# Performance work log

Hardware: AMD Instinct MI355X
Metric: run time of the kernel (lower is better)

## Reference

```python
import jax, jax.numpy as jnp
import numpy as np

B, T, D, H = 1024, 200, 128, 128


def setup_inputs() -> dict:
    key = jax.random.key(0)
    k1, k2, k3, k4 = jax.random.split(key, 4)
    item_his_eb = jax.random.normal(k1, (B, T, D), dtype=jnp.float32)
    seq_len = jax.random.randint(k2, (B,), 0, T, dtype=jnp.int32)
    # TF GRUCell packs [r, u] gates in one matmul over concat([x, h]).
    W_gate = jax.random.normal(k3, (D + H, 2 * H), dtype=jnp.float32) * (1.0 / np.sqrt(D + H))
    b_gate = jnp.ones((2 * H,), dtype=jnp.float32)  # TF GRUCell bias init = 1.0
    W_cand = jax.random.normal(k4, (D + H, H), dtype=jnp.float32) * (1.0 / np.sqrt(D + H))
    b_cand = jnp.zeros((H,), dtype=jnp.float32)
    return {"item_his_eb": item_his_eb, "seq_len": seq_len,
            "W_gate": W_gate, "b_gate": b_gate,
            "W_cand": W_cand, "b_cand": b_cand}


def reference(item_his_eb, seq_len, W_gate, b_gate, W_cand, b_cand):
    # dynamic_rnn(GRUCell(H)) with sequence_length masking.
    # Outputs are zero and state is held for steps t >= seq_len.
    Bq, Tq, Dq = item_his_eb.shape
    Hq = W_cand.shape[1]
    x_tbd = jnp.transpose(item_his_eb, (1, 0, 2))  # [T, B, D]

    def step(h, inp):
        x_t, t = inp  # x_t: [B, D], t: scalar int
        gates = jax.nn.sigmoid(jnp.concatenate([x_t, h], axis=-1) @ W_gate + b_gate)
        r, u = jnp.split(gates, 2, axis=-1)  # each [B, H]
        c = jnp.tanh(jnp.concatenate([x_t, r * h], axis=-1) @ W_cand + b_cand)
        h_new = u * h + (1.0 - u) * c
        valid = (t < seq_len)[:, None]  # [B, 1]
        h_next = jnp.where(valid, h_new, h)
        y = jnp.where(valid, h_new, jnp.zeros_like(h_new))
        return h_next, y

    h0 = jnp.zeros((Bq, Hq), dtype=item_his_eb.dtype)
    _, ys = jax.lax.scan(step, h0, (x_tbd, jnp.arange(Tq)))
    return jnp.transpose(ys, (1, 0, 2))  # [B, T, H]
```

## Files before the change

### kernel.cpp

```cpp
#include <hip/hip_runtime.h>

#define T_SZ 200
#define H_SZ 128

typedef __attribute__((ext_vector_type(8))) short    bf16x8;
typedef __attribute__((ext_vector_type(4))) float    f32x4;
typedef __attribute__((ext_vector_type(4))) int      i32x4;
typedef __attribute__((ext_vector_type(2))) unsigned u32x2;

__device__ __forceinline__ unsigned short f2bf(float f) {
  unsigned u = __builtin_bit_cast(unsigned, f);
  u += 0x7fffu + ((u >> 16) & 1u);
  return (unsigned short)(u >> 16);
}
__device__ __forceinline__ unsigned cvt_pk_bf16(float a, float b) {
  unsigned r;
  asm("v_cvt_pk_bf16_f32 %0, %1, %2" : "=v"(r) : "v"(a), "v"(b));
  return r;
}
__device__ __forceinline__ float sigmoid_fast(float x) {
  float e = __builtin_amdgcn_exp2f(-1.442695041f * x);
  return __builtin_amdgcn_rcpf(1.0f + e);
}
__device__ __forceinline__ float tanh_fast(float x) {
  float e = __builtin_amdgcn_exp2f(2.885390082f * x);
  return 1.0f - 2.0f * __builtin_amdgcn_rcpf(e + 1.0f);
}
__device__ __forceinline__ void ldsbar() {
  __asm__ __volatile__("" ::: "memory");
  __builtin_amdgcn_s_waitcnt(0xc07f);
  __builtin_amdgcn_s_barrier();
  __asm__ __volatile__("" ::: "memory");
}

__global__ __launch_bounds__(512, 1) void gru_fused(
    const float* __restrict__ X,
    const int*   __restrict__ seq_len,
    const float* __restrict__ Wg,
    const float* __restrict__ bg,
    const float* __restrict__ Wc,
    const float* __restrict__ bc,
    float* __restrict__ Y)
{
  __shared__ unsigned short hA[16 * 136];
  __shared__ unsigned short rhA[16 * 136];
  __shared__ unsigned short xA[2][16 * 136];

  const int tid  = threadIdx.x;
  const int lane = tid & 63;
  const int w    = tid >> 6;
  const int m16  = lane & 15;
  const int q    = lane >> 4;

  bf16x8 wgf[2][8];
  float  gbias[2];
  #pragma unroll
  for (int nt = 0; nt < 2; ++nt) {
    int col = nt * 128 + w * 16 + m16;
    gbias[nt] = bg[col];
    #pragma unroll
    for (int kb = 0; kb < 8; ++kb) {
      bf16x8 f;
      #pragma unroll
      for (int j = 0; j < 8; ++j)
        f[j] = (short)f2bf(Wg[(size_t)(kb * 32 + q * 8 + j) * 256 + col]);
      wgf[nt][kb] = f;
    }
  }
  const int colc = w * 16 + m16;
  bf16x8 wcf[8];
  float  cbias = bc[colc];
  #pragma unroll
  for (int kb = 0; kb < 8; ++kb) {
    bf16x8 f;
    #pragma unroll
    for (int j = 0; j < 8; ++j)
      f[j] = (short)f2bf(Wc[(size_t)(kb * 32 + q * 8 + j) * 128 + colc]);
    wcf[kb] = f;
  }

  const int bt = blockIdx.x;
  int slen[4];
  #pragma unroll
  for (int i = 0; i < 4; ++i) slen[i] = seq_len[bt * 16 + q * 4 + i];

  float h[4] = {0.f, 0.f, 0.f, 0.f};

  for (int idx = tid; idx < 16 * 136; idx += 512) hA[idx] = 0;

  const int xrow = tid >> 5;
  const int xk4  = (tid & 31) * 4;
  const float* xbase = X + (size_t)(bt * 16 + xrow) * T_SZ * 128 + xk4;

  auto xload = [&](int t, f32x4& r) {
    r = *(const f32x4*)(xbase + (size_t)t * 128);
  };
  auto xstage = [&](int buf, const f32x4& r) {
    unsigned d0 = cvt_pk_bf16(r.x, r.y);
    unsigned d1 = cvt_pk_bf16(r.z, r.w);
    *(u32x2*)&xA[buf][xrow * 136 + xk4] = (u32x2){d0, d1};
  };

  f32x4 x0r, x1r, xrE, xrO;
  xload(0, x0r); xload(1, x1r);
  xstage(0, x0r); xstage(1, x1r);
  xload(2, xrE); xload(3, xrO);
  ldsbar();

  f32x4 axrA, axuA, ccA, axrB, axuB, ccB;
  {
    bf16x8 xaf[4];
    #pragma unroll
    for (int kb = 0; kb < 4; ++kb)
      xaf[kb] = __builtin_bit_cast(bf16x8, *(const i32x4*)&xA[0][m16 * 136 + kb * 32 + q * 8]);
    f32x4 cc = { cbias, cbias, cbias, cbias };
    f32x4 ar = { gbias[0], gbias[0], gbias[0], gbias[0] };
    f32x4 au = { gbias[1], gbias[1], gbias[1], gbias[1] };
    #pragma unroll
    for (int kb = 0; kb < 4; ++kb) {
      cc = __builtin_amdgcn_mfma_f32_16x16x32_bf16(xaf[kb], wcf[kb],    cc, 0, 0, 0);
      ar = __builtin_amdgcn_mfma_f32_16x16x32_bf16(xaf[kb], wgf[0][kb], ar, 0, 0, 0);
      au = __builtin_amdgcn_mfma_f32_16x16x32_bf16(xaf[kb], wgf[1][kb], au, 0, 0, 0);
    }
    ccA = cc; axrA = ar; axuA = au;
  }
  ldsbar();

  float* const ybase = Y + (size_t)(bt * 16 + q * 4) * T_SZ * H_SZ + colc;

  auto step = [&](int t, f32x4& xreg,
                  f32x4& axin_r, f32x4& axin_u, f32x4& ccin,
                  f32x4& axout_r, f32x4& axout_u, f32x4& ccout) {
    bf16x8 haf[4];
    #pragma unroll
    for (int kb = 0; kb < 4; ++kb)
      haf[kb] = __builtin_bit_cast(bf16x8, *(const i32x4*)&hA[m16 * 136 + kb * 32 + q * 8]);

    if (t < 198) xstage(t & 1, xreg);
    if (t < 196) xload(t + 4, xreg);

    f32x4 ra = axin_r, rb = { 0.f, 0.f, 0.f, 0.f };
    ra = __builtin_amdgcn_mfma_f32_16x16x32_bf16(haf[0], wgf[0][4], ra, 0, 0, 0);
    ra = __builtin_amdgcn_mfma_f32_16x16x32_bf16(haf[1], wgf[0][5], ra, 0, 0, 0);
    rb = __builtin_amdgcn_mfma_f32_16x16x32_bf16(haf[2], wgf[0][6], rb, 0, 0, 0);
    rb = __builtin_amdgcn_mfma_f32_16x16x32_bf16(haf[3], wgf[0][7], rb, 0, 0, 0);

    float rh0 = sigmoid_fast(ra[0] + rb[0]) * h[0];
    float rh1 = sigmoid_fast(ra[1] + rb[1]) * h[1];
    float rh2 = sigmoid_fast(ra[2] + rb[2]) * h[2];
    float rh3 = sigmoid_fast(ra[3] + rb[3]) * h[3];
    unsigned rp01 = cvt_pk_bf16(rh0, rh1);
    unsigned rp23 = cvt_pk_bf16(rh2, rh3);
    rhA[(q * 4 + 0) * 136 + colc] = (unsigned short)(rp01 & 0xffffu);
    rhA[(q * 4 + 1) * 136 + colc] = (unsigned short)(rp01 >> 16);
    rhA[(q * 4 + 2) * 136 + colc] = (unsigned short)(rp23 & 0xffffu);
    rhA[(q * 4 + 3) * 136 + colc] = (unsigned short)(rp23 >> 16);
    ldsbar();

    bf16x8 rhf[4];
    #pragma unroll
    for (int kb = 0; kb < 4; ++kb)
      rhf[kb] = __builtin_bit_cast(bf16x8, *(const i32x4*)&rhA[m16 * 136 + kb * 32 + q * 8]);
    bf16x8 xaf2[4];
    if (t < 199) {
      const unsigned short* xb = xA[(t + 1) & 1];
      #pragma unroll
      for (int kb = 0; kb < 4; ++kb)
        xaf2[kb] = __builtin_bit_cast(bf16x8, *(const i32x4*)&xb[m16 * 136 + kb * 32 + q * 8]);
    }

    f32x4 ua = axin_u, ub = { 0.f, 0.f, 0.f, 0.f };
    ua = __builtin_amdgcn_mfma_f32_16x16x32_bf16(haf[0], wgf[1][4], ua, 0, 0, 0);
    ua = __builtin_amdgcn_mfma_f32_16x16x32_bf16(haf[1], wgf[1][5], ua, 0, 0, 0);
    ub = __builtin_amdgcn_mfma_f32_16x16x32_bf16(haf[2], wgf[1][6], ub, 0, 0, 0);
    ub = __builtin_amdgcn_mfma_f32_16x16x32_bf16(haf[3], wgf[1][7], ub, 0, 0, 0);

    f32x4 ca = ccin, cb = { 0.f, 0.f, 0.f, 0.f };
    ca = __builtin_amdgcn_mfma_f32_16x16x32_bf16(rhf[0], wcf[4], ca, 0, 0, 0);
    ca = __builtin_amdgcn_mfma_f32_16x16x32_bf16(rhf[1], wcf[5], ca, 0, 0, 0);
    cb = __builtin_amdgcn_mfma_f32_16x16x32_bf16(rhf[2], wcf[6], cb, 0, 0, 0);
    cb = __builtin_amdgcn_mfma_f32_16x16x32_bf16(rhf[3], wcf[7], cb, 0, 0, 0);

    if (t < 199) {
      f32x4 cc = { cbias, cbias, cbias, cbias };
      f32x4 ar = { gbias[0], gbias[0], gbias[0], gbias[0] };
      f32x4 au = { gbias[1], gbias[1], gbias[1], gbias[1] };
      #pragma unroll
      for (int kb = 0; kb < 4; ++kb) {
        cc = __builtin_amdgcn_mfma_f32_16x16x32_bf16(xaf2[kb], wcf[kb],    cc, 0, 0, 0);
        ar = __builtin_amdgcn_mfma_f32_16x16x32_bf16(xaf2[kb], wgf[0][kb], ar, 0, 0, 0);
        au = __builtin_amdgcn_mfma_f32_16x16x32_bf16(xaf2[kb], wgf[1][kb], au, 0, 0, 0);
      }
      ccout = cc; axout_r = ar; axout_u = au;
    }

    f32x4 uv;
    #pragma unroll
    for (int i = 0; i < 4; ++i) uv[i] = sigmoid_fast(ua[i] + ub[i]);

    #pragma unroll
    for (int i = 0; i < 4; ++i) {
      float c  = tanh_fast(ca[i] + cb[i]);
      float hn = uv[i] * (h[i] - c) + c;
      bool valid = (t < slen[i]);
      float hvz = valid ? hn : h[i];
      h[i] = hvz;
      ybase[(size_t)i * T_SZ * H_SZ + (size_t)t * H_SZ] = valid ? hn : 0.0f;
    }
    unsigned hp01 = cvt_pk_bf16(h[0], h[1]);
    unsigned hp23 = cvt_pk_bf16(h[2], h[3]);
    hA[(q * 4 + 0) * 136 + colc] = (unsigned short)(hp01 & 0xffffu);
    hA[(q * 4 + 1) * 136 + colc] = (unsigned short)(hp01 >> 16);
    hA[(q * 4 + 2) * 136 + colc] = (unsigned short)(hp23 & 0xffffu);
    hA[(q * 4 + 3) * 136 + colc] = (unsigned short)(hp23 >> 16);
    ldsbar();
  };

  for (int t = 0; t < 200; t += 2) {
    step(t,     xrE, axrA, axuA, ccA, axrB, axuB, ccB);
    step(t + 1, xrO, axrB, axuB, ccB, axrA, axuA, ccA);
  }
}

extern "C" void kernel_launch(void* const* d_in, const int* in_sizes, int n_in,
                              void* d_out, int out_size, void* d_ws, size_t ws_size,
                              hipStream_t stream) {
  const float* X   = (const float*)d_in[0];
  const int*   seq = (const int*)  d_in[1];
  const float* Wg  = (const float*)d_in[2];
  const float* bg  = (const float*)d_in[3];
  const float* Wc  = (const float*)d_in[4];
  const float* bc  = (const float*)d_in[5];
  float* Y = (float*)d_out;
  (void)d_ws; (void)ws_size;

  hipLaunchKernelGGL(gru_fused, dim3(64), dim3(512), 0, stream,
                     X, seq, Wg, bg, Wc, bc, Y);
}
```

Baseline: 334.2 us.

## Load X directly into MFMA fragment registers, dropping LDS staging

Each lane now reads its own MFMA A-fragment of X straight from global memory, prefetching two steps ahead, and converts it to bf16 in registers. This removes the shared-memory x buffers, the per-step LDS store and load of x, and the ping-pong accumulator sets. The update-gate accumulation is also merged into one chain instead of two partial sums. In exchange, global loads are no longer coalesced across rows (each lane reads 32-byte pieces), each thread holds more registers for the prefetched X, and the update-gate MFMA chain is longer and more serial.

```diff
diff --git a/kernel.cpp b/kernel.cpp
--- a/kernel.cpp
+++ b/kernel.cpp
@@ -6,7 +6,6 @@
 typedef __attribute__((ext_vector_type(8))) short    bf16x8;
 typedef __attribute__((ext_vector_type(4))) float    f32x4;
 typedef __attribute__((ext_vector_type(4))) int      i32x4;
-typedef __attribute__((ext_vector_type(2))) unsigned u32x2;
 
 __device__ __forceinline__ unsigned short f2bf(float f) {
   unsigned u = __builtin_bit_cast(unsigned, f);
@@ -44,7 +43,6 @@
 {
   __shared__ unsigned short hA[16 * 136];
   __shared__ unsigned short rhA[16 * 136];
-  __shared__ unsigned short xA[2][16 * 136];
 
   const int tid  = threadIdx.x;
   const int lane = tid & 63;
@@ -88,58 +86,58 @@
 
   for (int idx = tid; idx < 16 * 136; idx += 512) hA[idx] = 0;
 
-  const int xrow = tid >> 5;
-  const int xk4  = (tid & 31) * 4;
-  const float* xbase = X + (size_t)(bt * 16 + xrow) * T_SZ * 128 + xk4;
-
-  auto xload = [&](int t, f32x4& r) {
-    r = *(const f32x4*)(xbase + (size_t)t * 128);
+  const float* const xrow = X + (size_t)(bt * 16 + m16) * T_SZ * 128 + q * 8;
+  f32x4 xf[8];
+  auto xissue = [&](int t) {
+    const float* p = xrow + (size_t)t * 128;
+    #pragma unroll
+    for (int kb = 0; kb < 4; ++kb) {
+      xf[2 * kb]     = *(const f32x4*)(p + kb * 32);
+      xf[2 * kb + 1] = *(const f32x4*)(p + kb * 32 + 4);
+    }
   };
-  auto xstage = [&](int buf, const f32x4& r) {
-    unsigned d0 = cvt_pk_bf16(r.x, r.y);
-    unsigned d1 = cvt_pk_bf16(r.z, r.w);
-    *(u32x2*)&xA[buf][xrow * 136 + xk4] = (u32x2){d0, d1};
+
+  f32x4 axr, axu, cc;
+
+  auto xproj = [&]() {
+    bf16x8 xbf[4];
+    #pragma unroll
+    for (int kb = 0; kb < 4; ++kb) {
+      i32x4 pk = { (int)cvt_pk_bf16(xf[2 * kb].x,     xf[2 * kb].y),
+                   (int)cvt_pk_bf16(xf[2 * kb].z,     xf[2 * kb].w),
+                   (int)cvt_pk_bf16(xf[2 * kb + 1].x, xf[2 * kb + 1].y),
+                   (int)cvt_pk_bf16(xf[2 * kb + 1].z, xf[2 * kb + 1].w) };
+      xbf[kb] = __builtin_bit_cast(bf16x8, pk);
+    }
+    f32x4 c_ = { cbias, cbias, cbias, cbias };
+    f32x4 r_ = { gbias[0], gbias[0], gbias[0], gbias[0] };
+    f32x4 u_ = { gbias[1], gbias[1], gbias[1], gbias[1] };
+    #pragma unroll
+    for (int kb = 0; kb < 4; ++kb) {
+      c_ = __builtin_amdgcn_mfma_f32_16x16x32_bf16(xbf[kb], wcf[kb],    c_, 0, 0, 0);
+      r_ = __builtin_amdgcn_mfma_f32_16x16x32_bf16(xbf[kb], wgf[0][kb], r_, 0, 0, 0);
+      u_ = __builtin_amdgcn_mfma_f32_16x16x32_bf16(xbf[kb], wgf[1][kb], u_, 0, 0, 0);
+    }
+    cc = c_; axr = r_; axu = u_;
   };
 
-  f32x4 x0r, x1r, xrE, xrO;
-  xload(0, x0r); xload(1, x1r);
-  xstage(0, x0r); xstage(1, x1r);
-  xload(2, xrE); xload(3, xrO);
+  xissue(0);
   ldsbar();
-
-  f32x4 axrA, axuA, ccA, axrB, axuB, ccB;
   {
-    bf16x8 xaf[4];
-    #pragma unroll
-    for (int kb = 0; kb < 4; ++kb)
-      xaf[kb] = __builtin_bit_cast(bf16x8, *(const i32x4*)&xA[0][m16 * 136 + kb * 32 + q * 8]);
-    f32x4 cc = { cbias, cbias, cbias, cbias };
-    f32x4 ar = { gbias[0], gbias[0], gbias[0], gbias[0] };
-    f32x4 au = { gbias[1], gbias[1], gbias[1], gbias[1] };
-    #pragma unroll
-    for (int kb = 0; kb < 4; ++kb) {
-      cc = __builtin_amdgcn_mfma_f32_16x16x32_bf16(xaf[kb], wcf[kb],    cc, 0, 0, 0);
-      ar = __builtin_amdgcn_mfma_f32_16x16x32_bf16(xaf[kb], wgf[0][kb], ar, 0, 0, 0);
-      au = __builtin_amdgcn_mfma_f32_16x16x32_bf16(xaf[kb], wgf[1][kb], au, 0, 0, 0);
-    }
-    ccA = cc; axrA = ar; axuA = au;
-  }
-  ldsbar();
+    bf16x8 dummy_guard;  (void)dummy_guard;
+  }
+  xproj();
+  xissue(1);
 
   float* const ybase = Y + (size_t)(bt * 16 + q * 4) * T_SZ * H_SZ + colc;
 
-  auto step = [&](int t, f32x4& xreg,
-                  f32x4& axin_r, f32x4& axin_u, f32x4& ccin,
-                  f32x4& axout_r, f32x4& axout_u, f32x4& ccout) {
+  for (int t = 0; t < 200; ++t) {
     bf16x8 haf[4];
     #pragma unroll
     for (int kb = 0; kb < 4; ++kb)
       haf[kb] = __builtin_bit_cast(bf16x8, *(const i32x4*)&hA[m16 * 136 + kb * 32 + q * 8]);
 
-    if (t < 198) xstage(t & 1, xreg);
-    if (t < 196) xload(t + 4, xreg);
-
-    f32x4 ra = axin_r, rb = { 0.f, 0.f, 0.f, 0.f };
+    f32x4 ra = axr, rb = { 0.f, 0.f, 0.f, 0.f };
     ra = __builtin_amdgcn_mfma_f32_16x16x32_bf16(haf[0], wgf[0][4], ra, 0, 0, 0);
     ra = __builtin_amdgcn_mfma_f32_16x16x32_bf16(haf[1], wgf[0][5], ra, 0, 0, 0);
     rb = __builtin_amdgcn_mfma_f32_16x16x32_bf16(haf[2], wgf[0][6], rb, 0, 0, 0);
@@ -161,42 +159,27 @@
     #pragma unroll
     for (int kb = 0; kb < 4; ++kb)
       rhf[kb] = __builtin_bit_cast(bf16x8, *(const i32x4*)&rhA[m16 * 136 + kb * 32 + q * 8]);
-    bf16x8 xaf2[4];
-    if (t < 199) {
-      const unsigned short* xb = xA[(t + 1) & 1];
-      #pragma unroll
-      for (int kb = 0; kb < 4; ++kb)
-        xaf2[kb] = __builtin_bit_cast(bf16x8, *(const i32x4*)&xb[m16 * 136 + kb * 32 + q * 8]);
-    }
-
-    f32x4 ua = axin_u, ub = { 0.f, 0.f, 0.f, 0.f };
+
+    f32x4 ua = axu;
     ua = __builtin_amdgcn_mfma_f32_16x16x32_bf16(haf[0], wgf[1][4], ua, 0, 0, 0);
     ua = __builtin_amdgcn_mfma_f32_16x16x32_bf16(haf[1], wgf[1][5], ua, 0, 0, 0);
-    ub = __builtin_amdgcn_mfma_f32_16x16x32_bf16(haf[2], wgf[1][6], ub, 0, 0, 0);
-    ub = __builtin_amdgcn_mfma_f32_16x16x32_bf16(haf[3], wgf[1][7], ub, 0, 0, 0);
-
-    f32x4 ca = ccin, cb = { 0.f, 0.f, 0.f, 0.f };
+    ua = __builtin_amdgcn_mfma_f32_16x16x32_bf16(haf[2], wgf[1][6], ua, 0, 0, 0);
+    ua = __builtin_amdgcn_mfma_f32_16x16x32_bf16(haf[3], wgf[1][7], ua, 0, 0, 0);
+
+    f32x4 ca = cc, cb = { 0.f, 0.f, 0.f, 0.f };
     ca = __builtin_amdgcn_mfma_f32_16x16x32_bf16(rhf[0], wcf[4], ca, 0, 0, 0);
     ca = __builtin_amdgcn_mfma_f32_16x16x32_bf16(rhf[1], wcf[5], ca, 0, 0, 0);
     cb = __builtin_amdgcn_mfma_f32_16x16x32_bf16(rhf[2], wcf[6], cb, 0, 0, 0);
     cb = __builtin_amdgcn_mfma_f32_16x16x32_bf16(rhf[3], wcf[7], cb, 0, 0, 0);
 
     if (t < 199) {
-      f32x4 cc = { cbias, cbias, cbias, cbias };
-      f32x4 ar = { gbias[0], gbias[0], gbias[0], gbias[0] };
-      f32x4 au = { gbias[1], gbias[1], gbias[1], gbias[1] };
-      #pragma unroll
-      for (int kb = 0; kb < 4; ++kb) {
-        cc = __builtin_amdgcn_mfma_f32_16x16x32_bf16(xaf2[kb], wcf[kb],    cc, 0, 0, 0);
-        ar = __builtin_amdgcn_mfma_f32_16x16x32_bf16(xaf2[kb], wgf[0][kb], ar, 0, 0, 0);
-        au = __builtin_amdgcn_mfma_f32_16x16x32_bf16(xaf2[kb], wgf[1][kb], au, 0, 0, 0);
-      }
-      ccout = cc; axout_r = ar; axout_u = au;
+      xproj();
+      if (t < 198) xissue(t + 2);
     }
 
     f32x4 uv;
     #pragma unroll
-    for (int i = 0; i < 4; ++i) uv[i] = sigmoid_fast(ua[i] + ub[i]);
+    for (int i = 0; i < 4; ++i) uv[i] = sigmoid_fast(ua[i]);
 
     #pragma unroll
     for (int i = 0; i < 4; ++i) {
@@ -214,11 +197,6 @@
     hA[(q * 4 + 2) * 136 + colc] = (unsigned short)(hp23 & 0xffffu);
     hA[(q * 4 + 3) * 136 + colc] = (unsigned short)(hp23 >> 16);
     ldsbar();
-  };
-
-  for (int t = 0; t < 200; t += 2) {
-    step(t,     xrE, axrA, axuA, ccA, axrB, axuB, ccB);
-    step(t + 1, xrO, axrB, axuB, ccB, axrA, axuA, ccA);
   }
 }
 
```

Result: slower. 670.1 us (+100.5%).

## Swap MFMA operands so each lane owns four hidden columns of one row

Applied to the files above, without the earlier changes.

The MFMA A/B operands are swapped so the accumulator holds a transposed tile: each lane now owns four consecutive hidden columns for a single batch row, not one column across four rows. This lets the per-step h and r*h LDS writes become single 8-byte stores, the Y output a single 16-byte vector store, and seq_len a single scalar per lane. The u-gate accumulation is also folded into one chain, removing one add per element but lengthening that dependency chain. Bias loading becomes vector loads matching the new layout.

```diff
diff --git a/kernel.cpp b/kernel.cpp
--- a/kernel.cpp
+++ b/kernel.cpp
@@ -53,11 +53,9 @@
   const int q    = lane >> 4;
 
   bf16x8 wgf[2][8];
-  float  gbias[2];
   #pragma unroll
   for (int nt = 0; nt < 2; ++nt) {
     int col = nt * 128 + w * 16 + m16;
-    gbias[nt] = bg[col];
     #pragma unroll
     for (int kb = 0; kb < 8; ++kb) {
       bf16x8 f;
@@ -69,7 +67,6 @@
   }
   const int colc = w * 16 + m16;
   bf16x8 wcf[8];
-  float  cbias = bc[colc];
   #pragma unroll
   for (int kb = 0; kb < 8; ++kb) {
     bf16x8 f;
@@ -79,10 +76,13 @@
     wcf[kb] = f;
   }
 
+  const int col4 = w * 16 + q * 4;
+  const f32x4 gbias_r = *(const f32x4*)&bg[col4];
+  const f32x4 gbias_u = *(const f32x4*)&bg[128 + col4];
+  const f32x4 cbias4  = *(const f32x4*)&bc[col4];
+
   const int bt = blockIdx.x;
-  int slen[4];
-  #pragma unroll
-  for (int i = 0; i < 4; ++i) slen[i] = seq_len[bt * 16 + q * 4 + i];
+  const int slen = seq_len[bt * 16 + m16];
 
   float h[4] = {0.f, 0.f, 0.f, 0.f};
 
@@ -113,20 +113,18 @@
     #pragma unroll
     for (int kb = 0; kb < 4; ++kb)
       xaf[kb] = __builtin_bit_cast(bf16x8, *(const i32x4*)&xA[0][m16 * 136 + kb * 32 + q * 8]);
-    f32x4 cc = { cbias, cbias, cbias, cbias };
-    f32x4 ar = { gbias[0], gbias[0], gbias[0], gbias[0] };
-    f32x4 au = { gbias[1], gbias[1], gbias[1], gbias[1] };
+    f32x4 cc = cbias4, ar = gbias_r, au = gbias_u;
     #pragma unroll
     for (int kb = 0; kb < 4; ++kb) {
-      cc = __builtin_amdgcn_mfma_f32_16x16x32_bf16(xaf[kb], wcf[kb],    cc, 0, 0, 0);
-      ar = __builtin_amdgcn_mfma_f32_16x16x32_bf16(xaf[kb], wgf[0][kb], ar, 0, 0, 0);
-      au = __builtin_amdgcn_mfma_f32_16x16x32_bf16(xaf[kb], wgf[1][kb], au, 0, 0, 0);
+      cc = __builtin_amdgcn_mfma_f32_16x16x32_bf16(wcf[kb],    xaf[kb], cc, 0, 0, 0);
+      ar = __builtin_amdgcn_mfma_f32_16x16x32_bf16(wgf[0][kb], xaf[kb], ar, 0, 0, 0);
+      au = __builtin_amdgcn_mfma_f32_16x16x32_bf16(wgf[1][kb], xaf[kb], au, 0, 0, 0);
     }
     ccA = cc; axrA = ar; axuA = au;
   }
   ldsbar();
 
-  float* const ybase = Y + (size_t)(bt * 16 + q * 4) * T_SZ * H_SZ + colc;
+  float* const ybase = Y + (size_t)(bt * 16 + m16) * T_SZ * H_SZ + col4;
 
   auto step = [&](int t, f32x4& xreg,
                   f32x4& axin_r, f32x4& axin_u, f32x4& ccin,
@@ -140,21 +138,17 @@
     if (t < 196) xload(t + 4, xreg);
 
     f32x4 ra = axin_r, rb = { 0.f, 0.f, 0.f, 0.f };
-    ra = __builtin_amdgcn_mfma_f32_16x16x32_bf16(haf[0], wgf[0][4], ra, 0, 0, 0);
-    ra = __builtin_amdgcn_mfma_f32_16x16x32_bf16(haf[1], wgf[0][5], ra, 0, 0, 0);
-    rb = __builtin_amdgcn_mfma_f32_16x16x32_bf16(haf[2], wgf[0][6], rb, 0, 0, 0);
-    rb = __builtin_amdgcn_mfma_f32_16x16x32_bf16(haf[3], wgf[0][7], rb, 0, 0, 0);
+    ra = __builtin_amdgcn_mfma_f32_16x16x32_bf16(wgf[0][4], haf[0], ra, 0, 0, 0);
+    ra = __builtin_amdgcn_mfma_f32_16x16x32_bf16(wgf[0][5], haf[1], ra, 0, 0, 0);
+    rb = __builtin_amdgcn_mfma_f32_16x16x32_bf16(wgf[0][6], haf[2], rb, 0, 0, 0);
+    rb = __builtin_amdgcn_mfma_f32_16x16x32_bf16(wgf[0][7], haf[3], rb, 0, 0, 0);
 
     float rh0 = sigmoid_fast(ra[0] + rb[0]) * h[0];
     float rh1 = sigmoid_fast(ra[1] + rb[1]) * h[1];
     float rh2 = sigmoid_fast(ra[2] + rb[2]) * h[2];
     float rh3 = sigmoid_fast(ra[3] + rb[3]) * h[3];
-    unsigned rp01 = cvt_pk_bf16(rh0, rh1);
-    unsigned rp23 = cvt_pk_bf16(rh2, rh3);
-    rhA[(q * 4 + 0) * 136 + colc] = (unsigned short)(rp01 & 0xffffu);
-    rhA[(q * 4 + 1) * 136 + colc] = (unsigned short)(rp01 >> 16);
-    rhA[(q * 4 + 2) * 136 + colc] = (unsigned short)(rp23 & 0xffffu);
-    rhA[(q * 4 + 3) * 136 + colc] = (unsigned short)(rp23 >> 16);
+    *(u32x2*)&rhA[m16 * 136 + col4] =
+        (u32x2){ cvt_pk_bf16(rh0, rh1), cvt_pk_bf16(rh2, rh3) };
     ldsbar();
 
     bf16x8 rhf[4];
@@ -169,50 +163,42 @@
         xaf2[kb] = __builtin_bit_cast(bf16x8, *(const i32x4*)&xb[m16 * 136 + kb * 32 + q * 8]);
     }
 
-    f32x4 ua = axin_u, ub = { 0.f, 0.f, 0.f, 0.f };
-    ua = __builtin_amdgcn_mfma_f32_16x16x32_bf16(haf[0], wgf[1][4], ua, 0, 0, 0);
-    ua = __builtin_amdgcn_mfma_f32_16x16x32_bf16(haf[1], wgf[1][5], ua, 0, 0, 0);
-    ub = __builtin_amdgcn_mfma_f32_16x16x32_bf16(haf[2], wgf[1][6], ub, 0, 0, 0);
-    ub = __builtin_amdgcn_mfma_f32_16x16x32_bf16(haf[3], wgf[1][7], ub, 0, 0, 0);
+    f32x4 ua = axin_u;
+    ua = __builtin_amdgcn_mfma_f32_16x16x32_bf16(wgf[1][4], haf[0], ua, 0, 0, 0);
+    ua = __builtin_amdgcn_mfma_f32_16x16x32_bf16(wgf[1][5], haf[1], ua, 0, 0, 0);
+    ua = __builtin_amdgcn_mfma_f32_16x16x32_bf16(wgf[1][6], haf[2], ua, 0, 0, 0);
+    ua = __builtin_amdgcn_mfma_f32_16x16x32_bf16(wgf[1][7], haf[3], ua, 0, 0, 0);
 
     f32x4 ca = ccin, cb = { 0.f, 0.f, 0.f, 0.f };
-    ca = __builtin_amdgcn_mfma_f32_16x16x32_bf16(rhf[0], wcf[4], ca, 0, 0, 0);
-    ca = __builtin_amdgcn_mfma_f32_16x16x32_bf16(rhf[1], wcf[5], ca, 0, 0, 0);
-    cb = __builtin_amdgcn_mfma_f32_16x16x32_bf16(rhf[2], wcf[6], cb, 0, 0, 0);
-    cb = __builtin_amdgcn_mfma_f32_16x16x32_bf16(rhf[3], wcf[7], cb, 0, 0, 0);
+    ca = __builtin_amdgcn_mfma_f32_16x16x32_bf16(wcf[4], rhf[0], ca, 0, 0, 0);
+    ca = __builtin_amdgcn_mfma_f32_16x16x32_bf16(wcf[5], rhf[1], ca, 0, 0, 0);
+    cb = __builtin_amdgcn_mfma_f32_16x16x32_bf16(wcf[6], rhf[2], cb, 0, 0, 0);
+    cb = __builtin_amdgcn_mfma_f32_16x16x32_bf16(wcf[7], rhf[3], cb, 0, 0, 0);
 
     if (t < 199) {
-      f32x4 cc = { cbias, cbias, cbias, cbias };
-      f32x4 ar = { gbias[0], gbias[0], gbias[0], gbias[0] };
-      f32x4 au = { gbias[1], gbias[1], gbias[1], gbias[1] };
+      f32x4 cc = cbias4, ar = gbias_r, au = gbias_u;
       #pragma unroll
       for (int kb = 0; kb < 4; ++kb) {
-        cc = __builtin_amdgcn_mfma_f32_16x16x32_bf16(xaf2[kb], wcf[kb],    cc, 0, 0, 0);
-        ar = __builtin_amdgcn_mfma_f32_16x16x32_bf16(xaf2[kb], wgf[0][kb], ar, 0, 0, 0);
-        au = __builtin_amdgcn_mfma_f32_16x16x32_bf16(xaf2[kb], wgf[1][kb], au, 0, 0, 0);
+        cc = __builtin_amdgcn_mfma_f32_16x16x32_bf16(wcf[kb],    xaf2[kb], cc, 0, 0, 0);
+        ar = __builtin_amdgcn_mfma_f32_16x16x32_bf16(wgf[0][kb], xaf2[kb], ar, 0, 0, 0);
+        au = __builtin_amdgcn_mfma_f32_16x16x32_bf16(wgf[1][kb], xaf2[kb], au, 0, 0, 0);
       }
       ccout = cc; axout_r = ar; axout_u = au;
     }
 
-    f32x4 uv;
-    #pragma unroll
-    for (int i = 0; i < 4; ++i) uv[i] = sigmoid_fast(ua[i] + ub[i]);
-
+    const bool valid = (t < slen);
+    f32x4 yv;
     #pragma unroll
     for (int i = 0; i < 4; ++i) {
+      float u  = sigmoid_fast(ua[i]);
       float c  = tanh_fast(ca[i] + cb[i]);
-      float hn = uv[i] * (h[i] - c) + c;
-      bool valid = (t < slen[i]);
-      float hvz = valid ? hn : h[i];
-      h[i] = hvz;
-      ybase[(size_t)i * T_SZ * H_SZ + (size_t)t * H_SZ] = valid ? hn : 0.0f;
-    }
-    unsigned hp01 = cvt_pk_bf16(h[0], h[1]);
-    unsigned hp23 = cvt_pk_bf16(h[2], h[3]);
-    hA[(q * 4 + 0) * 136 + colc] = (unsigned short)(hp01 & 0xffffu);
-    hA[(q * 4 + 1) * 136 + colc] = (unsigned short)(hp01 >> 16);
-    hA[(q * 4 + 2) * 136 + colc] = (unsigned short)(hp23 & 0xffffu);
-    hA[(q * 4 + 3) * 136 + colc] = (unsigned short)(hp23 >> 16);
+      float hn = u * (h[i] - c) + c;
+      h[i]  = valid ? hn : h[i];
+      yv[i] = valid ? hn : 0.0f;
+    }
+    *(f32x4*)(ybase + (size_t)t * H_SZ) = yv;
+    *(u32x2*)&hA[m16 * 136 + col4] =
+        (u32x2){ cvt_pk_bf16(h[0], h[1]), cvt_pk_bf16(h[2], h[3]) };
     ldsbar();
   };
 
```

After: 324.4 us. 2.9% less time.
